# Optimization experiments

Hardware: AMD Instinct MI355X
Metric: run time of the kernel (lower is better)

## Reference

```python
import jax, jax.numpy as jnp
import numpy as np
from jax import lax

# --- module constants (from init_kwargs) ---
A_COEF = 0.7
B_COEF = 0.0
RADIUS = 8
EPS = 1e-3
EPS_LOG = 1e-6
EPS_SCALE = 1e-4
DOWN = 0.5
KSIZE = 2 * RADIUS + 1


def _sep_box_filter(x4):
    """Separable box filter on [1,1,H,W] with reflect padding (matches torch)."""
    p = jnp.pad(x4, ((0, 0), (0, 0), (RADIUS, RADIUS), (RADIUS, RADIUS)), mode='reflect')
    box_h = jnp.full((1, 1, 1, KSIZE), 1.0 / KSIZE, dtype=x4.dtype)
    box_v = jnp.full((1, 1, KSIZE, 1), 1.0 / KSIZE, dtype=x4.dtype)
    h = lax.conv(p, box_h, (1, 1), 'VALID')
    return lax.conv(h, box_v, (1, 1), 'VALID')


def _guided_filter(I2d):
    """Self-guided filter on [H,W] (guide == input)."""
    I4 = I2d[None, None]
    mean_I = _sep_box_filter(I4)
    mean_II = _sep_box_filter(I4 * I4)
    var_I = mean_II - mean_I * mean_I
    a = var_I / (var_I + EPS)
    b = mean_I - a * mean_I
    mean_a = _sep_box_filter(a)
    mean_b = _sep_box_filter(b)
    out = mean_a * I4 + mean_b
    return out[0, 0]


def _resize_bilinear(img, out_h, out_w):
    """Bilinear resize of [H,W], torch align_corners=False semantics (no antialias)."""
    in_h, in_w = img.shape
    ys = jnp.clip((jnp.arange(out_h, dtype=jnp.float32) + 0.5) * (in_h / out_h) - 0.5,
                  0.0, in_h - 1.0)
    xs = jnp.clip((jnp.arange(out_w, dtype=jnp.float32) + 0.5) * (in_w / out_w) - 0.5,
                  0.0, in_w - 1.0)
    y0 = jnp.floor(ys).astype(jnp.int32)
    x0 = jnp.floor(xs).astype(jnp.int32)
    y1 = jnp.minimum(y0 + 1, in_h - 1)
    x1 = jnp.minimum(x0 + 1, in_w - 1)
    wy = (ys - y0)[:, None]  # [out_h,1]
    wx = (xs - x0)[None, :]  # [1,out_w]
    Ia = img[y0][:, x0]
    Ib = img[y0][:, x1]
    Ic = img[y1][:, x0]
    Id = img[y1][:, x1]
    top = Ia * (1.0 - wx) + Ib * wx
    bot = Ic * (1.0 - wx) + Id * wx
    return top * (1.0 - wy) + bot * wy


def setup_inputs() -> dict:
    key = jax.random.key(0)
    x = jax.random.uniform(key, (2160, 3840, 3), dtype=jnp.float32)  # RGB in [0,1]
    return {"x": x}


def reference(x) -> jnp.ndarray:
    H, W = x.shape[0], x.shape[1]
    R, G, B = x[..., 0], x[..., 1], x[..., 2]
    Y = 0.2126 * R + 0.7152 * G + 0.0722 * B
    Y_log = jnp.log2(jnp.maximum(Y, EPS_LOG))

    # downsample -> guided filter -> upsample (DOWN < 1.0 path)
    dh, dw = int(H * DOWN), int(W * DOWN)
    Y_log_down = _resize_bilinear(Y_log, dh, dw)
    Y_base_down = _guided_filter(Y_log_down)
    Y_base = _resize_bilinear(Y_base_down, H, W)

    Y_detail = Y_log - Y_base
    Y_tm = (A_COEF * Y_base + B_COEF) + Y_detail
    Y_out = jnp.exp2(Y_tm)
    scale = Y_out / (Y + EPS_SCALE)
    out = x * scale[..., None]
    return jnp.clip(out, 0.0, 1.0)
```

## Files before the change

kernel.cpp:

```cpp
#include <hip/hip_runtime.h>

#define FH 2160
#define FW 3840
#define DH 1080
#define DW 1920
#define RAD 8
#define KS 17
#define INV_KS (1.0f / 17.0f)
#define EPS_GF 1e-3f
#define EPS_LOG 1e-6f
#define EPS_SCALE 1e-4f
#define A_COEF 0.7f

#define TS 32
#define IT 48
#define ITP 50
#define NT1 2040
#define TPX1 255

#define ATR 34
#define ATC 50
#define ATP2 52
#define BTC 34
#define BTR 18
#define BTP 35
#define NT2 4080
#define TPX2 510

__device__ __forceinline__ int refl(int p, int n) {
    p = (p < 0) ? -p : p;
    return (p >= n) ? (2 * n - 2 - p) : p;
}

__device__ __forceinline__ float luma3(float r, float g, float b) {
    return 0.2126f * r + 0.7152f * g + 0.0722f * b;
}

__global__ void __launch_bounds__(256)
k_gf_front(const float* __restrict__ x, float* __restrict__ Dg,
           float2* __restrict__ ABg) {
    __shared__ float inD[IT * ITP];
    __shared__ float2 hh[IT * TS];
    int bid = blockIdx.x;
    int swz = (bid & 7) * TPX1 + (bid >> 3);
    int bx = swz % 60, by = swz / 60;
    int tx0 = bx * TS, ty0 = by * TS;
    int t = threadIdx.x;

    for (int s = t; s < IT * IT; s += 256) {
        int li = s / IT, lj = s - li * IT;
        int gi = refl(ty0 - RAD + li, DH);
        int gj = refl(tx0 - RAD + lj, DW);
        const float* p0 = x + ((size_t)(2 * gi) * FW + (size_t)(2 * gj)) * 3;
        const float* p1 = p0 + (size_t)FW * 3;
        float2 a0 = *(const float2*)(p0);
        float2 a1 = *(const float2*)(p0 + 2);
        float2 a2 = *(const float2*)(p0 + 4);
        float2 b0 = *(const float2*)(p1);
        float2 b1 = *(const float2*)(p1 + 2);
        float2 b2 = *(const float2*)(p1 + 4);
        float y00 = fmaxf(luma3(a0.x, a0.y, a1.x), EPS_LOG);
        float y01 = fmaxf(luma3(a1.y, a2.x, a2.y), EPS_LOG);
        float y10 = fmaxf(luma3(b0.x, b0.y, b1.x), EPS_LOG);
        float y11 = fmaxf(luma3(b1.y, b2.x, b2.y), EPS_LOG);
        inD[li * ITP + lj] = 0.25f * __log2f((y00 * y01) * (y10 * y11));
    }
    __syncthreads();

    for (int task = t; task < IT * 8; task += 256) {
        int r = task >> 3, c0 = (task & 7) * 4;
        const float* row = &inD[r * ITP + c0];
        const float2* row2 = (const float2*)row;
        float s1 = 0.f, s2 = 0.f;
#pragma unroll
        for (int k = 0; k < 8; ++k) {
            float2 p = row2[k];
            s1 += p.x + p.y;
            s2 += p.x * p.x + p.y * p.y;
        }
        float v16 = row[16];
        s1 += v16; s2 += v16 * v16;
        int base = r * TS + c0;
        hh[base] = make_float2(s1 * INV_KS, s2 * INV_KS);
#pragma unroll
        for (int cc = 1; cc < 4; ++cc) {
            float vo = row[cc - 1], vi = row[cc + 16];
            s1 += vi - vo;
            s2 += vi * vi - vo * vo;
            hh[base + cc] = make_float2(s1 * INV_KS, s2 * INV_KS);
        }
    }
    __syncthreads();

    {
        int rs = t >> 5, c = t & 31;
        int r0 = rs * 4;
        float sx = 0.f, sy = 0.f;
#pragma unroll
        for (int k = 0; k < KS; ++k) {
            float2 h = hh[(r0 + k) * TS + c];
            sx += h.x; sy += h.y;
        }
#pragma unroll
        for (int rr = 0; rr < 4; ++rr) {
            int r = r0 + rr;
            if (rr > 0) {
                float2 hi = hh[(r + 16) * TS + c];
                float2 ho = hh[(r - 1) * TS + c];
                sx += hi.x - ho.x;
                sy += hi.y - ho.y;
            }
            int gi = ty0 + r;
            if (gi < DH) {
                float mI = sx * INV_KS, mII = sy * INV_KS;
                float var = mII - mI * mI;
                float av = var / (var + EPS_GF);
                size_t g = (size_t)gi * DW + tx0 + c;
                ABg[g] = make_float2(av, mI - av * mI);
                Dg[g] = inD[(r + RAD) * ITP + c + RAD];
            }
        }
    }
}

__global__ void __launch_bounds__(256)
k_gf_back(const float* __restrict__ x, const float2* __restrict__ ABg,
          const float* __restrict__ Dg, float* __restrict__ out) {
    __shared__ float2 inAB[ATR * ATP2];
    __shared__ float2 hAB[ATR * BTC];
    __shared__ float baseT[BTR * BTP];
    int bid = blockIdx.x;
    int swz = (bid & 7) * TPX2 + (bid >> 3);
    int bx = swz % 60, by = swz / 60;
    int ox0 = bx * 64, oy0 = by * 32;
    int bh0 = by * 16 - 1, bw0 = bx * 32 - 1;
    int ah0 = bh0 - RAD, aw0 = bw0 - RAD;
    int t = threadIdx.x;

    for (int s = t; s < ATR * ATC; s += 256) {
        int li = s / ATC, lj = s - li * ATC;
        inAB[li * ATP2 + lj] = ABg[(size_t)refl(ah0 + li, DH) * DW + refl(aw0 + lj, DW)];
    }
    __syncthreads();

    for (int task = t; task < ATR * 9; task += 256) {
        int r = task / 9, c0 = (task - r * 9) * 4;
        const float2* row = &inAB[r * ATP2 + c0];
        float s1 = 0.f, s2 = 0.f;
#pragma unroll
        for (int k = 0; k < KS; ++k) { float2 v = row[k]; s1 += v.x; s2 += v.y; }
        int base = r * BTC + c0;
#pragma unroll
        for (int cc = 0; cc < 4; ++cc) {
            if (cc > 0) {
                float2 vi = row[cc + 16], vo = row[cc - 1];
                s1 += vi.x - vo.x;
                s2 += vi.y - vo.y;
            }
            if (c0 + cc < BTC) hAB[base + cc] = make_float2(s1 * INV_KS, s2 * INV_KS);
        }
    }
    __syncthreads();

    for (int task = t; task < 5 * BTC; task += 256) {
        int rs = task / BTC, c = task - rs * BTC;
        int r0 = rs * 4;
        int sz = (rs == 4) ? 2 : 4;
        float s1 = 0.f, s2 = 0.f;
#pragma unroll
        for (int k = 0; k < KS; ++k) {
            float2 v = hAB[(r0 + k) * BTC + c];
            s1 += v.x; s2 += v.y;
        }
        for (int rr = 0; rr < sz; ++rr) {
            int r = r0 + rr;
            if (rr > 0) {
                float2 vi = hAB[(r + 16) * BTC + c];
                float2 vo = hAB[(r - 1) * BTC + c];
                s1 += vi.x - vo.x;
                s2 += vi.y - vo.y;
            }
            size_t g = (size_t)refl(bh0 + r, DH) * DW + refl(bw0 + c, DW);
            baseT[r * BTP + c] = (s1 * INV_KS) * Dg[g] + s2 * INV_KS;
        }
    }
    __syncthreads();

    for (int q = t; q < 32 * 16; q += 256) {
        int qi = q >> 4, qj = q & 15;
        int oy = oy0 + qi;
        if (oy < FH) {
            float ys = fminf(fmaxf((oy + 0.5f) * 0.5f - 0.5f, 0.f), (float)(DH - 1));
            int y0 = (int)ys;
            int y1 = min(y0 + 1, DH - 1);
            float wy = ys - (float)y0;
            const float* br0 = &baseT[(y0 - bh0) * BTP];
            const float* br1 = &baseT[(y1 - bh0) * BTP];

            size_t off = ((size_t)oy * FW + (size_t)(ox0 + 4 * qj)) * 3;
            const float4* xin = (const float4*)(x + off);
            float4 v0 = xin[0], v1 = xin[1], v2 = xin[2];
            float px[12] = {v0.x, v0.y, v0.z, v0.w, v1.x, v1.y, v1.z, v1.w,
                            v2.x, v2.y, v2.z, v2.w};
            float po[12];
#pragma unroll
            for (int p = 0; p < 4; ++p) {
                int ox = ox0 + 4 * qj + p;
                float xs = fminf(fmaxf((ox + 0.5f) * 0.5f - 0.5f, 0.f), (float)(DW - 1));
                int x0 = (int)xs;
                int x1 = min(x0 + 1, DW - 1);
                float wx = xs - (float)x0;
                int c0 = x0 - bw0, c1 = x1 - bw0;
                float top = br0[c0] * (1.f - wx) + br0[c1] * wx;
                float bot = br1[c0] * (1.f - wx) + br1[c1] * wx;
                float Yb = top * (1.f - wy) + bot * wy;

                float cr = px[3 * p], cg = px[3 * p + 1], cb = px[3 * p + 2];
                float Y = luma3(cr, cg, cb);
                float Ylog = __log2f(fmaxf(Y, EPS_LOG));
                float Yout = exp2f(A_COEF * Yb + (Ylog - Yb));
                float sc = Yout / (Y + EPS_SCALE);
                po[3 * p + 0] = fminf(fmaxf(cr * sc, 0.f), 1.f);
                po[3 * p + 1] = fminf(fmaxf(cg * sc, 0.f), 1.f);
                po[3 * p + 2] = fminf(fmaxf(cb * sc, 0.f), 1.f);
            }
            float4* op = (float4*)(out + off);
            op[0] = make_float4(po[0], po[1], po[2], po[3]);
            op[1] = make_float4(po[4], po[5], po[6], po[7]);
            op[2] = make_float4(po[8], po[9], po[10], po[11]);
        }
    }
}

extern "C" void kernel_launch(void* const* d_in, const int* in_sizes, int n_in,
                              void* d_out, int out_size, void* d_ws, size_t ws_size,
                              hipStream_t stream) {
    const float* x = (const float*)d_in[0];
    float* out = (float*)d_out;
    float* ws = (float*)d_ws;
    const size_t DN = (size_t)DW * DH;

    float* D = ws;
    float2* AB = (float2*)(ws + DN);

    k_gf_front<<<dim3(NT1), dim3(256), 0, stream>>>(x, D, AB);
    k_gf_back <<<dim3(NT2), dim3(256), 0, stream>>>(x, AB, D, out);
}
```

Before: 71.74 us.

## Prefetch epilogue pixels early, specialize bilinear upsample weights, fast reciprocals

The back kernel now issues its full-resolution RGB loads at kernel start, so their latency overlaps the shared-memory box filtering. The exact-2x bilinear upsample is rewritten with fixed 0.25/0.75 weights and precomputed column indices, which removes the per-pixel float index math. Interior tiles get a reflect-free AB load path. Divisions are replaced by hardware rcp approximations in both kernels. The cost is higher register pressure from holding 24 floats across the barriers, and rcp is slightly less accurate than a true divide.

```diff
diff --git a/kernel.cpp b/kernel.cpp
--- a/kernel.cpp
+++ b/kernel.cpp
@@ -114,13 +114,62 @@
             if (gi < DH) {
                 float mI = sx * INV_KS, mII = sy * INV_KS;
                 float var = mII - mI * mI;
-                float av = var / (var + EPS_GF);
+                float av = var * __builtin_amdgcn_rcpf(var + EPS_GF);
                 size_t g = (size_t)gi * DW + tx0 + c;
                 ABg[g] = make_float2(av, mI - av * mI);
                 Dg[g] = inD[(r + RAD) * ITP + c + RAD];
             }
         }
     }
+}
+
+__device__ __forceinline__ void epi_quad(int oy, int qi,
+                                         int jm1, int j0, int jp1, int jp2,
+                                         const float* baseT,
+                                         float4 v0, float4 v1, float4 v2,
+                                         float* __restrict__ out, size_t off) {
+    int ny = oy >> 1;
+    int h = qi >> 1;
+    int rA, rB;
+    float wA, wB;
+    if (oy & 1) {
+        rA = h + 1;
+        rB = (ny + 1 <= DH - 1) ? h + 2 : h + 1;
+        wA = 0.75f; wB = 0.25f;
+    } else {
+        rA = (ny >= 1) ? h : h + 1;
+        rB = h + 1;
+        wA = 0.25f; wB = 0.75f;
+    }
+    const float* brA = &baseT[rA * BTP];
+    const float* brB = &baseT[rB * BTP];
+    float Vm1 = wA * brA[jm1] + wB * brB[jm1];
+    float V0  = wA * brA[j0]  + wB * brB[j0];
+    float Vp1 = wA * brA[jp1] + wB * brB[jp1];
+    float Vp2 = wA * brA[jp2] + wB * brB[jp2];
+    float Ybs[4] = {0.25f * Vm1 + 0.75f * V0,
+                    0.75f * V0  + 0.25f * Vp1,
+                    0.25f * V0  + 0.75f * Vp1,
+                    0.75f * Vp1 + 0.25f * Vp2};
+    float px[12] = {v0.x, v0.y, v0.z, v0.w, v1.x, v1.y, v1.z, v1.w,
+                    v2.x, v2.y, v2.z, v2.w};
+    float po[12];
+#pragma unroll
+    for (int p = 0; p < 4; ++p) {
+        float cr = px[3 * p], cg = px[3 * p + 1], cb = px[3 * p + 2];
+        float Y = luma3(cr, cg, cb);
+        float Ylog = __log2f(fmaxf(Y, EPS_LOG));
+        float Yb = Ybs[p];
+        float Yout = exp2f(A_COEF * Yb + (Ylog - Yb));
+        float sc = Yout * __builtin_amdgcn_rcpf(Y + EPS_SCALE);
+        po[3 * p + 0] = fminf(fmaxf(cr * sc, 0.f), 1.f);
+        po[3 * p + 1] = fminf(fmaxf(cg * sc, 0.f), 1.f);
+        po[3 * p + 2] = fminf(fmaxf(cb * sc, 0.f), 1.f);
+    }
+    float4* op = (float4*)(out + off);
+    op[0] = make_float4(po[0], po[1], po[2], po[3]);
+    op[1] = make_float4(po[4], po[5], po[6], po[7]);
+    op[2] = make_float4(po[8], po[9], po[10], po[11]);
 }
 
 __global__ void __launch_bounds__(256)
@@ -137,9 +186,27 @@
     int ah0 = bh0 - RAD, aw0 = bw0 - RAD;
     int t = threadIdx.x;
 
-    for (int s = t; s < ATR * ATC; s += 256) {
-        int li = s / ATC, lj = s - li * ATC;
-        inAB[li * ATP2 + lj] = ABg[(size_t)refl(ah0 + li, DH) * DW + refl(aw0 + lj, DW)];
+    int qi0 = t >> 4, qj = t & 15;
+    int oy_0 = oy0 + qi0;
+    int oy_1 = oy_0 + 16;
+    size_t off0 = ((size_t)oy_0 * FW + (size_t)(ox0 + 4 * qj)) * 3;
+    size_t off1 = (oy_1 < FH) ? ((size_t)oy_1 * FW + (size_t)(ox0 + 4 * qj)) * 3 : off0;
+    const float4* xin0 = (const float4*)(x + off0);
+    const float4* xin1 = (const float4*)(x + off1);
+    float4 xa0 = xin0[0], xa1 = xin0[1], xa2 = xin0[2];
+    float4 xb0 = xin1[0], xb1 = xin1[1], xb2 = xin1[2];
+
+    if (ah0 >= 0 && ah0 + ATR <= DH && aw0 >= 0 && aw0 + ATC <= DW) {
+        const float2* src = ABg + (size_t)ah0 * DW + aw0;
+        for (int s = t; s < ATR * ATC; s += 256) {
+            int li = s / ATC, lj = s - li * ATC;
+            inAB[li * ATP2 + lj] = src[(size_t)li * DW + lj];
+        }
+    } else {
+        for (int s = t; s < ATR * ATC; s += 256) {
+            int li = s / ATC, lj = s - li * ATC;
+            inAB[li * ATP2 + lj] = ABg[(size_t)refl(ah0 + li, DH) * DW + refl(aw0 + lj, DW)];
+        }
     }
     __syncthreads();
 
@@ -186,49 +253,15 @@
     }
     __syncthreads();
 
-    for (int q = t; q < 32 * 16; q += 256) {
-        int qi = q >> 4, qj = q & 15;
-        int oy = oy0 + qi;
-        if (oy < FH) {
-            float ys = fminf(fmaxf((oy + 0.5f) * 0.5f - 0.5f, 0.f), (float)(DH - 1));
-            int y0 = (int)ys;
-            int y1 = min(y0 + 1, DH - 1);
-            float wy = ys - (float)y0;
-            const float* br0 = &baseT[(y0 - bh0) * BTP];
-            const float* br1 = &baseT[(y1 - bh0) * BTP];
-
-            size_t off = ((size_t)oy * FW + (size_t)(ox0 + 4 * qj)) * 3;
-            const float4* xin = (const float4*)(x + off);
-            float4 v0 = xin[0], v1 = xin[1], v2 = xin[2];
-            float px[12] = {v0.x, v0.y, v0.z, v0.w, v1.x, v1.y, v1.z, v1.w,
-                            v2.x, v2.y, v2.z, v2.w};
-            float po[12];
-#pragma unroll
-            for (int p = 0; p < 4; ++p) {
-                int ox = ox0 + 4 * qj + p;
-                float xs = fminf(fmaxf((ox + 0.5f) * 0.5f - 0.5f, 0.f), (float)(DW - 1));
-                int x0 = (int)xs;
-                int x1 = min(x0 + 1, DW - 1);
-                float wx = xs - (float)x0;
-                int c0 = x0 - bw0, c1 = x1 - bw0;
-                float top = br0[c0] * (1.f - wx) + br0[c1] * wx;
-                float bot = br1[c0] * (1.f - wx) + br1[c1] * wx;
-                float Yb = top * (1.f - wy) + bot * wy;
-
-                float cr = px[3 * p], cg = px[3 * p + 1], cb = px[3 * p + 2];
-                float Y = luma3(cr, cg, cb);
-                float Ylog = __log2f(fmaxf(Y, EPS_LOG));
-                float Yout = exp2f(A_COEF * Yb + (Ylog - Yb));
-                float sc = Yout / (Y + EPS_SCALE);
-                po[3 * p + 0] = fminf(fmaxf(cr * sc, 0.f), 1.f);
-                po[3 * p + 1] = fminf(fmaxf(cg * sc, 0.f), 1.f);
-                po[3 * p + 2] = fminf(fmaxf(cb * sc, 0.f), 1.f);
-            }
-            float4* op = (float4*)(out + off);
-            op[0] = make_float4(po[0], po[1], po[2], po[3]);
-            op[1] = make_float4(po[4], po[5], po[6], po[7]);
-            op[2] = make_float4(po[8], po[9], po[10], po[11]);
-        }
+    {
+        int mq = bx * 32 + 2 * qj;
+        int jm1 = max(mq - 1, 0) - bw0;
+        int j0 = mq - bw0;
+        int jp1 = min(mq + 1, DW - 1) - bw0;
+        int jp2 = min(mq + 2, DW - 1) - bw0;
+        epi_quad(oy_0, qi0, jm1, j0, jp1, jp2, baseT, xa0, xa1, xa2, out, off0);
+        if (oy_1 < FH)
+            epi_quad(oy_1, qi0 + 16, jm1, j0, jp1, jp2, baseT, xb0, xb1, xb2, out, off1);
     }
 }
 
```

Result: slower. 77.36 us (+7.8%).
